# Kernel tuning notes

Hardware: AMD Instinct MI355X
Metric: run time of the kernel (lower is better)

## Reference

```python
import jax, jax.numpy as jnp
import numpy as np

LAMDA = 0.1    # regularization strength
ALPHA = 1.0    # proximal weighting (default forward arg)
TAU = 0.25     # Chambolle step size
MAX_ITER = 50
TOL = 1e-4


def _gradient(x):
    # forward differences with zero padding at the far boundary -> (2, H, W)
    gx = jnp.pad(x[1:, :] - x[:-1, :], ((0, 1), (0, 0)))
    gy = jnp.pad(x[:, 1:] - x[:, :-1], ((0, 0), (0, 1)))
    return jnp.stack((gx, gy), axis=0)


def _divergence(p):
    # matches torch: pad(p[:-1]-p[1:], 1 at the leading boundary)
    dx = jnp.pad(p[0][:-1, :] - p[0][1:, :], ((1, 0), (0, 0)))
    dy = jnp.pad(p[1][:, :-1] - p[1][:, 1:], ((0, 0), (1, 0)))
    return dx + dy


def setup_inputs() -> dict:
    key = jax.random.key(0)
    x = jax.random.normal(key, (4096, 4096), dtype=jnp.float32)
    return {"x": x}


def reference(x):
    def body(carry, _):
        p, done = carry
        g = _gradient(x - ALPHA * LAMDA * _divergence(p))
        p_new = jnp.clip(p + TAU * g, -1.0, 1.0)  # l1 norm projection
        dp_max = jnp.max(jnp.abs(p_new - p))
        # emulate the early break: freeze p once converged
        p_next = jnp.where(done, p, p_new)
        done = done | (dp_max < TOL)
        return (p_next, done), None

    p0 = jnp.zeros((2,) + x.shape, dtype=x.dtype)
    (p, _), _ = jax.lax.scan(body, (p0, jnp.array(False)), None, length=MAX_ITER)
    return x - ALPHA * LAMDA * _divergence(p)
```

## Files before the change

kernel.cpp:

```cpp
#include <hip/hip_runtime.h>
#include <hip/hip_fp16.h>

#define HH 4096
#define WW 4096

constexpr float C_LAM = 0.1f;
constexpr float TAU_F = 0.25f;

#define BX 64
#define BY 8
#define VEC 4
#define TILE_W (BX * VEC)

#define TW2 64
#define TH2 32
#define ERR 36
#define ECC 72
#define NCH (ECC / 4)
#define NSL (ERR * NCH)
#define LSZ (ERR * ECC)

#define TH8 32
#define TW8 64
#define XC8 80
#define NS8 12
#define NQ8 10
#define NT8 120

typedef float    __attribute__((ext_vector_type(4))) f32x4_t;
typedef float    __attribute__((ext_vector_type(2))) f32x2_t;
typedef unsigned __attribute__((ext_vector_type(2))) u32x2_t;

union H2x4 { float4 f4; f32x4_t v4; __half2 h2[4]; unsigned u32[4]; };
union H2x2 { float2 f2; f32x2_t v2; __half2 h2[2]; unsigned u32[2]; };
union H2U  { __half2 h; unsigned int u; };

__device__ __forceinline__ float clip1(float v) {
    return fminf(1.0f, fmaxf(-1.0f, v));
}

__device__ __forceinline__ unsigned h2u(__half2 h) { H2U a; a.h = h; return a.u; }
__device__ __forceinline__ __half2  u2h(unsigned u){ H2U a; a.u = u; return a.h; }

__device__ __forceinline__ __half2 permh(__half2 a, __half2 b, unsigned sel) {
    unsigned d;
    asm("v_perm_b32 %0, %1, %2, %3" : "=v"(d) : "v"(h2u(a)), "v"(h2u(b)), "v"(sel));
    return u2h(d);
}
__device__ __forceinline__ __half2 andh(__half2 v, unsigned m) { return u2h(h2u(v) & m); }

__device__ __forceinline__ __half2 clamp1h2(__half2 v) {
    H2U a; a.h = v;
    unsigned int lo = 0xBC00BC00u;
    unsigned int hi = 0x3C003C00u;
    unsigned int t, r;
    asm("v_pk_max_f16 %0, %1, %2" : "=v"(t) : "v"(a.u), "v"(lo));
    asm("v_pk_min_f16 %0, %1, %2" : "=v"(r) : "v"(t),   "v"(hi));
    H2U b; b.u = r;
    return b.h;
}

__device__ __forceinline__ __half2 shfl_up_h2(__half2 v) {
    H2U a; a.h = v;
    int s = __shfl_up((int)a.u, 1, 64);
    H2U b; b.u = (unsigned)s;
    return b.h;
}

__device__ __forceinline__ __half2 align16(__half2 hi, __half2 lo) {
    H2U a, b, d;
    a.h = hi; b.h = lo;
    asm("v_alignbit_b32 %0, %1, %2, 16" : "=v"(d.u) : "v"(a.u), "v"(b.u));
    return d.h;
}

__global__ __launch_bounds__(512) void tv_first(const float* __restrict__ x,
                                                __half2* __restrict__ po,
                                                __half* __restrict__ xh)
{
    const int tx = threadIdx.x, ty = threadIdx.y;
    const int i = blockIdx.y * BY + ty;
    const int j = blockIdx.x * TILE_W + tx * VEC;
    const size_t idx = (size_t)i * WW + j;

    float4 xc4 = *(const float4*)(x + idx);
    float4 xd4 = make_float4(0.f, 0.f, 0.f, 0.f);
    if (i < HH - 1) xd4 = *(const float4*)(x + idx + WW);

    float c[4] = {xc4.x, xc4.y, xc4.z, xc4.w};
    float d[4] = {xd4.x, xd4.y, xd4.z, xd4.w};

    float xr = __shfl_down(c[0], 1, 64);
    if (tx == BX - 1 && j + VEC < WW) xr = x[idx + VEC];

    H2x4 o;
#pragma unroll
    for (int e = 0; e < 4; ++e) {
        float gx = (i < HH - 1) ? (d[e] - c[e]) : 0.f;
        float rn = (e < 3) ? c[e + 1] : xr;
        float gy = (j + e < WW - 1) ? (rn - c[e]) : 0.f;
        o.h2[e] = __floats2half2_rn(clip1(TAU_F * gx), clip1(TAU_F * gy));
    }
    *(float4*)(po + idx) = o.f4;

    H2x2 xs;
    xs.h2[0] = __floats2half2_rn(c[0], c[1]);
    xs.h2[1] = __floats2half2_rn(c[2], c[3]);
    *(float2*)(xh + idx) = xs.f2;
}

template<bool EDGE>
__device__ __forceinline__ void iter8_body(const __half* __restrict__ xh,
                                           const __half2* __restrict__ pi,
                                           __half2* __restrict__ po,
                                           __half* pxB, __half* uT,
                                           unsigned* pyE, unsigned* uE)
{
    const int tid = threadIdx.x;
    const bool act = (tid < NT8);
    const int t = act ? tid : (NT8 - 1);
    const int s = t / NQ8;
    const int q = t - s * NQ8;
    const int r0 = blockIdx.y * TH8, c0 = blockIdx.x * TW8;
    const int gi0 = r0 - 8 + 4 * s;
    const int gj0 = c0 - 8 + 8 * q;
    const int gjc = EDGE ? min(max(gj0, 0), WW - 8) : gj0;

    const int lB  = s * XC8 + 8 * q;
    const int lBu = ((s > 0) ? (s - 1) : 0) * XC8 + 8 * q;
    const int lBd = ((s < NS8 - 1) ? (s + 1) : s) * XC8 + 8 * q;
    const int eO = t * 2;
    const int eL = ((q > 0) ? (t - 1) : t) * 2;
    const int eR = ((q < NQ8 - 1) ? (t + 1) : t) * 2;
    const bool wout = act && (s >= 2) && (s <= 9) && (q >= 1) && (q <= 8);

    unsigned mdy = 0xFFFFFFFFu, mgy = 0xFFFFFFFFu;
    if (EDGE) {
        if (gj0 == 0)      mdy = 0xFFFF0000u;
        if (gj0 + 8 == WW) mgy = 0x0000FFFFu;
    }

    const __half2 tau2 = __float2half2_rn(TAU_F);
    const __half2 nC2  = __float2half2_rn(-C_LAM);
    const unsigned SEL0 = 0x05040100u;
    const unsigned SELH = 0x07060302u;
    const unsigned SELM = 0x05040302u;

    __half2 X[4][4], Y[4][4], XHr[4][4], U[4][4];

#pragma unroll
    for (int k = 0; k < 4; ++k) {
        int gik = gi0 + k;
        if (EDGE) gik = min(max(gik, 0), HH - 1);
        const size_t go = (size_t)gik * WW + gjc;
        H2x4 v0; v0.v4 = *(const f32x4_t*)(pi + go);
        H2x4 v1; v1.v4 = *(const f32x4_t*)(pi + go + 4);
        H2x4 xv; xv.v4 = *(const f32x4_t*)(xh + go);
        X[k][0] = permh(v0.h2[1], v0.h2[0], SEL0);
        Y[k][0] = permh(v0.h2[1], v0.h2[0], SELH);
        X[k][1] = permh(v0.h2[3], v0.h2[2], SEL0);
        Y[k][1] = permh(v0.h2[3], v0.h2[2], SELH);
        X[k][2] = permh(v1.h2[1], v1.h2[0], SEL0);
        Y[k][2] = permh(v1.h2[1], v1.h2[0], SELH);
        X[k][3] = permh(v1.h2[3], v1.h2[2], SEL0);
        Y[k][3] = permh(v1.h2[3], v1.h2[2], SELH);
#pragma unroll
        for (int m = 0; m < 4; ++m) XHr[k][m] = xv.h2[m];
    }

    auto publish = [&]() {
        if (act) {
            H2x4 w;
#pragma unroll
            for (int m = 0; m < 4; ++m) w.h2[m] = X[3][m];
            *(f32x4_t*)(pxB + lB) = w.v4;
            u32x2_t e;
            e.x = h2u(permh(Y[1][3], Y[0][3], SELH));
            e.y = h2u(permh(Y[3][3], Y[2][3], SELH));
            *(u32x2_t*)(pyE + eO) = e;
        }
    };

    auto ustage = [&]() {
        H2x4 pu; pu.v4 = *(const f32x4_t*)(pxB + lBu);
        u32x2_t Lp = *(const u32x2_t*)(pyE + eL);
        const __half2 L0 = u2h(Lp.x), L1 = u2h(Lp.y);
#pragma unroll
        for (int k = 0; k < 4; ++k) {
            __half2 dx[4], zm[4], dy[4];
#pragma unroll
            for (int m = 0; m < 4; ++m)
                dx[m] = __hsub2((k == 0) ? pu.h2[m] : X[k - 1][m], X[k][m]);
            if (EDGE && !(gi0 + k > 0)) {
#pragma unroll
                for (int m = 0; m < 4; ++m) dx[m] = u2h(0u);
            }
            zm[0] = (k == 0) ? permh(Y[k][0], L0, SEL0)
                  : (k == 1) ? permh(Y[k][0], L0, SELM)
                  : (k == 2) ? permh(Y[k][0], L1, SEL0)
                             : permh(Y[k][0], L1, SELM);
            zm[1] = align16(Y[k][1], Y[k][0]);
            zm[2] = align16(Y[k][2], Y[k][1]);
            zm[3] = align16(Y[k][3], Y[k][2]);
#pragma unroll
            for (int m = 0; m < 4; ++m) dy[m] = __hsub2(zm[m], Y[k][m]);
            if (EDGE) dy[0] = andh(dy[0], mdy);
#pragma unroll
            for (int m = 0; m < 4; ++m)
                U[k][m] = __hfma2(__hadd2(dx[m], dy[m]), nC2, XHr[k][m]);
        }
        if (act) {
            H2x4 w;
#pragma unroll
            for (int m = 0; m < 4; ++m) w.h2[m] = U[0][m];
            *(f32x4_t*)(uT + lB) = w.v4;
            u32x2_t e;
            e.x = h2u(permh(U[1][0], U[0][0], SEL0));
            e.y = h2u(permh(U[3][0], U[2][0], SEL0));
            *(u32x2_t*)(uE + eO) = e;
        }
    };

    auto pstage = [&]() {
        H2x4 ud; ud.v4 = *(const f32x4_t*)(uT + lBd);
        u32x2_t Rp = *(const u32x2_t*)(uE + eR);
        const __half2 R0 = u2h(Rp.x), R1 = u2h(Rp.y);
#pragma unroll
        for (int k = 0; k < 4; ++k) {
            __half2 gx[4], zp[4], gy[4];
#pragma unroll
            for (int m = 0; m < 4; ++m)
                gx[m] = __hsub2((k == 3) ? ud.h2[m] : U[k + 1][m], U[k][m]);
            if (EDGE && !(gi0 + k < HH - 1)) {
#pragma unroll
                for (int m = 0; m < 4; ++m) gx[m] = u2h(0u);
            }
            zp[0] = align16(U[k][1], U[k][0]);
            zp[1] = align16(U[k][2], U[k][1]);
            zp[2] = align16(U[k][3], U[k][2]);
            zp[3] = (k == 0) ? permh(R0, U[k][3], SELM)
                  : (k == 1) ? permh(R0, U[k][3], SELH)
                  : (k == 2) ? permh(R1, U[k][3], SELM)
                             : permh(R1, U[k][3], SELH);
#pragma unroll
            for (int m = 0; m < 4; ++m) gy[m] = __hsub2(zp[m], U[k][m]);
            if (EDGE) gy[3] = andh(gy[3], mgy);
#pragma unroll
            for (int m = 0; m < 4; ++m) {
                X[k][m] = clamp1h2(__hfma2(gx[m], tau2, X[k][m]));
                Y[k][m] = clamp1h2(__hfma2(gy[m], tau2, Y[k][m]));
            }
        }
    };

#pragma unroll 1
    for (int it = 0; it < 7; ++it) {
        publish(); __syncthreads();
        ustage();  __syncthreads();
        pstage();
    }
    publish(); __syncthreads();
    ustage();  __syncthreads();
    pstage();

    if (wout) {
#pragma unroll
        for (int k = 0; k < 4; ++k) {
            const size_t go = (size_t)(gi0 + k) * WW + gj0;
            H2x4 w0, w1;
            w0.h2[0] = permh(Y[k][0], X[k][0], SEL0);
            w0.h2[1] = permh(Y[k][0], X[k][0], SELH);
            w0.h2[2] = permh(Y[k][1], X[k][1], SEL0);
            w0.h2[3] = permh(Y[k][1], X[k][1], SELH);
            w1.h2[0] = permh(Y[k][2], X[k][2], SEL0);
            w1.h2[1] = permh(Y[k][2], X[k][2], SELH);
            w1.h2[2] = permh(Y[k][3], X[k][3], SEL0);
            w1.h2[3] = permh(Y[k][3], X[k][3], SELH);
            *(f32x4_t*)(po + go)     = w0.v4;
            *(f32x4_t*)(po + go + 4) = w1.v4;
        }
    }
}

__global__ __launch_bounds__(128, 4) void tv_iter8(const __half* __restrict__ xh,
                                                   const __half2* __restrict__ pi,
                                                   __half2* __restrict__ po)
{
    __shared__ __align__(16) __half   pxB[NS8 * XC8];
    __shared__ __align__(16) __half   uT [NS8 * XC8];
    __shared__ __align__(8)  unsigned pyE[NT8 * 2];
    __shared__ __align__(8)  unsigned uE [NT8 * 2];

    const bool edge = (blockIdx.x == 0) || (blockIdx.x == gridDim.x - 1) ||
                      (blockIdx.y == 0) || (blockIdx.y == gridDim.y - 1);
    if (!edge) iter8_body<false>(xh, pi, po, pxB, uT, pyE, uE);
    else       iter8_body<true >(xh, pi, po, pxB, uT, pyE, uE);
}

__global__ __launch_bounds__(256) void tv_last(const __half* __restrict__ xh,
                                               const float* __restrict__ x,
                                               const __half2* __restrict__ pi,
                                               float* __restrict__ out)
{
    __shared__ __half2 sp0[LSZ];
    __shared__ __half2 sp1[LSZ];
    __shared__ float   su [LSZ];

    const int tid  = threadIdx.x;
    const int lane = tid & 63;
    const int r0 = blockIdx.y * TH2;
    const int c0 = blockIdx.x * TW2;
    const __half2 tau2 = __float2half2_rn(TAU_F);

    int lb[3], lup[3], llf[3], ldn[3], lrt[3], gj0a[3], gofs[3];
    bool wr[3];
#pragma unroll
    for (int r = 0; r < 3; ++r) {
        int slot = tid + 256 * r;
        wr[r] = (slot < NSL);
        if (slot >= NSL) slot = NSL - 1;
        int cr = slot / NCH;
        int cc = slot - cr * NCH;
        int gi  = r0 - 2 + cr;
        int gj0 = c0 - 4 + cc * 4;
        int gic = min(max(gi, 0), HH - 1);
        int gjc = min(max(gj0, 0), WW - 4);
        gofs[r] = gic * WW + gjc;
        int l   = cr * ECC + cc * 4;
        lb[r]  = l;
        lup[r] = (cr > 0) ? l - ECC : l;
        llf[r] = (l > 0) ? l - 1 : 0;
        ldn[r] = (cr < ERR - 1) ? l + ECC : l;
        lrt[r] = min(l + 4, LSZ - 1);
        gj0a[r] = gj0;
    }

    __half2 c2[3][4];
    H2x2    xc[3];
#pragma unroll
    for (int r = 0; r < 3; ++r) {
        H2x4 v; v.f4 = *(const float4*)(pi + gofs[r]);
        xc[r].f2    = *(const float2*)(xh + gofs[r]);
        if (wr[r]) *(float4*)&sp0[lb[r]] = v.f4;
        c2[r][0] = v.h2[0]; c2[r][1] = v.h2[1];
        c2[r][2] = v.h2[2]; c2[r][3] = v.h2[3];
    }
    __syncthreads();

    float u1v[3][4];
#pragma unroll
    for (int r = 0; r < 3; ++r) {
        H2x4 up; up.f4 = *(float4*)&sp0[lup[r]];
        __half2 lf = shfl_up_h2(c2[r][3]);
        if (lane == 0) lf = sp0[llf[r]];
        float xs[4] = {__low2float(xc[r].h2[0]), __high2float(xc[r].h2[0]),
                       __low2float(xc[r].h2[1]), __high2float(xc[r].h2[1])};
        float4 w;
        float* wp = &w.x;
#pragma unroll
        for (int e = 0; e < 4; ++e) {
            __half2 cc = c2[r][e];
            __half2 le = (e == 0) ? lf : c2[r][e - 1];
            float dx = __low2float(up.h2[e]) - __low2float(cc);
            float dy = __high2float(le) - __high2float(cc);
            dy = (gj0a[r] + e > 0) ? dy : 0.f;
            float u = xs[e] - C_LAM * (dx + dy);
            u1v[r][e] = u;
            wp[e] = u;
        }
        if (wr[r]) *(float4*)&su[lb[r]] = w;
    }
    __syncthreads();

#pragma unroll
    for (int r = 0; r < 3; ++r) {
        float4 dn4 = *(float4*)&su[ldn[r]];
        float urr = __shfl_down(u1v[r][0], 1, 64);
        if (lane == 63) urr = su[lrt[r]];
        float dn[4] = {dn4.x, dn4.y, dn4.z, dn4.w};
        H2x4 w;
#pragma unroll
        for (int e = 0; e < 4; ++e) {
            float uc = u1v[r][e];
            float gx = dn[e] - uc;
            float rt = (e == 3) ? urr : u1v[r][e + 1];
            float gy = (gj0a[r] + e < WW - 1) ? (rt - uc) : 0.f;
            __half2 g = __float22half2_rn(make_float2(gx, gy));
            w.h2[e] = clamp1h2(__hfma2(g, tau2, c2[r][e]));
        }
        if (wr[r]) *(float4*)&sp1[lb[r]] = w.f4;
    }
    __syncthreads();

#pragma unroll
    for (int r = 0; r < 2; ++r) {
        int slot = tid + 256 * r;
        int ir = slot >> 4, icc = slot & 15;
        int er = ir + 2, ec = icc * 4 + 4;
        int l  = er * ECC + ec;
        int gi = r0 + ir, gj = c0 + icc * 4;

        H2x4 pc_; pc_.f4 = *(float4*)&sp1[l];
        H2x4 pu_; pu_.f4 = *(float4*)&sp1[l - ECC];
        __half2 plf = shfl_up_h2(pc_.h2[3]);
        if ((tid & 15) == 0) plf = sp1[l - 1];

        float4 xr4 = *(const float4*)(x + (size_t)gi * WW + gj);
        float xv[4] = {xr4.x, xr4.y, xr4.z, xr4.w};
        float o[4];
#pragma unroll
        for (int e = 0; e < 4; ++e) {
            __half2 cc = pc_.h2[e];
            __half2 le = (e == 0) ? plf : pc_.h2[e - 1];
            float dx = __low2float(pu_.h2[e]) - __low2float(cc);
            dx = (gi > 0) ? dx : 0.f;
            float dy = __high2float(le) - __high2float(cc);
            dy = (gj + e > 0) ? dy : 0.f;
            o[e] = xv[e] - C_LAM * (dx + dy);
        }
        *(float4*)(out + (size_t)gi * WW + gj) = make_float4(o[0], o[1], o[2], o[3]);
    }
}

extern "C" void kernel_launch(void* const* d_in, const int* in_sizes, int n_in,
                              void* d_out, int out_size, void* d_ws, size_t ws_size,
                              hipStream_t stream)
{
    const float* x = (const float*)d_in[0];
    float* out = (float*)d_out;
    const size_t N = (size_t)HH * (size_t)WW;

    __half2* pA = (__half2*)d_ws;
    __half2* pB = pA + N;
    __half*  xh = (__half*)(pB + N);

    dim3 b1(BX, BY), g1(WW / TILE_W, HH / BY);
    dim3 b8(128),    g8(WW / TW8, HH / TH8);
    dim3 bL(256),    gL(WW / TW2, HH / TH2);

    tv_first<<<g1, b1, 0, stream>>>(x, pA, xh);
    __half2 *pin = pA, *pout = pB;
    for (int p = 0; p < 6; ++p) {
        tv_iter8<<<g8, b8, 0, stream>>>(xh, pin, pout);
        __half2* t = pin; pin = pout; pout = t;
    }
    tv_last<<<gL, bL, 0, stream>>>(xh, x, pin, out);
}
```

Before: 506.0 us.

## Halve rows per thread in fused 8-iteration kernel, doubling block threads

Each thread of the temporally-blocked 8-iteration kernel now owns 2 rows instead of 4, so the block grows from 128 to 256 threads (240 active), with shared edge buffers shrunk to one word per thread. The goal is to cut per-thread register pressure and expose more parallel waves per tile to hide latency. In exchange there are more shared-memory halo exchanges relative to compute, and the occupancy hint in launch bounds is dropped.

```diff
diff --git a/kernel.cpp b/kernel.cpp
--- a/kernel.cpp
+++ b/kernel.cpp
@@ -23,13 +23,12 @@
 #define TH8 32
 #define TW8 64
 #define XC8 80
-#define NS8 12
+#define NS8 24
 #define NQ8 10
-#define NT8 120
+#define NT8 240
 
 typedef float    __attribute__((ext_vector_type(4))) f32x4_t;
 typedef float    __attribute__((ext_vector_type(2))) f32x2_t;
-typedef unsigned __attribute__((ext_vector_type(2))) u32x2_t;
 
 union H2x4 { float4 f4; f32x4_t v4; __half2 h2[4]; unsigned u32[4]; };
 union H2x2 { float2 f2; f32x2_t v2; __half2 h2[2]; unsigned u32[2]; };
@@ -122,17 +121,17 @@
     const int s = t / NQ8;
     const int q = t - s * NQ8;
     const int r0 = blockIdx.y * TH8, c0 = blockIdx.x * TW8;
-    const int gi0 = r0 - 8 + 4 * s;
+    const int gi0 = r0 - 8 + 2 * s;
     const int gj0 = c0 - 8 + 8 * q;
     const int gjc = EDGE ? min(max(gj0, 0), WW - 8) : gj0;
 
     const int lB  = s * XC8 + 8 * q;
     const int lBu = ((s > 0) ? (s - 1) : 0) * XC8 + 8 * q;
     const int lBd = ((s < NS8 - 1) ? (s + 1) : s) * XC8 + 8 * q;
-    const int eO = t * 2;
-    const int eL = ((q > 0) ? (t - 1) : t) * 2;
-    const int eR = ((q < NQ8 - 1) ? (t + 1) : t) * 2;
-    const bool wout = act && (s >= 2) && (s <= 9) && (q >= 1) && (q <= 8);
+    const int eO = t;
+    const int eL = (q > 0) ? (t - 1) : t;
+    const int eR = (q < NQ8 - 1) ? (t + 1) : t;
+    const bool wout = act && (s >= 4) && (s < 20) && (q >= 1) && (q <= 8);
 
     unsigned mdy = 0xFFFFFFFFu, mgy = 0xFFFFFFFFu;
     if (EDGE) {
@@ -146,10 +145,10 @@
     const unsigned SELH = 0x07060302u;
     const unsigned SELM = 0x05040302u;
 
-    __half2 X[4][4], Y[4][4], XHr[4][4], U[4][4];
-
-#pragma unroll
-    for (int k = 0; k < 4; ++k) {
+    __half2 X[2][4], Y[2][4], XHr[2][4], U[2][4];
+
+#pragma unroll
+    for (int k = 0; k < 2; ++k) {
         int gik = gi0 + k;
         if (EDGE) gik = min(max(gik, 0), HH - 1);
         const size_t go = (size_t)gik * WW + gjc;
@@ -172,33 +171,27 @@
         if (act) {
             H2x4 w;
 #pragma unroll
-            for (int m = 0; m < 4; ++m) w.h2[m] = X[3][m];
+            for (int m = 0; m < 4; ++m) w.h2[m] = X[1][m];
             *(f32x4_t*)(pxB + lB) = w.v4;
-            u32x2_t e;
-            e.x = h2u(permh(Y[1][3], Y[0][3], SELH));
-            e.y = h2u(permh(Y[3][3], Y[2][3], SELH));
-            *(u32x2_t*)(pyE + eO) = e;
+            pyE[eO] = h2u(permh(Y[1][3], Y[0][3], SELH));
         }
     };
 
     auto ustage = [&]() {
         H2x4 pu; pu.v4 = *(const f32x4_t*)(pxB + lBu);
-        u32x2_t Lp = *(const u32x2_t*)(pyE + eL);
-        const __half2 L0 = u2h(Lp.x), L1 = u2h(Lp.y);
-#pragma unroll
-        for (int k = 0; k < 4; ++k) {
+        const __half2 L = u2h(pyE[eL]);
+#pragma unroll
+        for (int k = 0; k < 2; ++k) {
             __half2 dx[4], zm[4], dy[4];
 #pragma unroll
             for (int m = 0; m < 4; ++m)
-                dx[m] = __hsub2((k == 0) ? pu.h2[m] : X[k - 1][m], X[k][m]);
+                dx[m] = __hsub2((k == 0) ? pu.h2[m] : X[0][m], X[k][m]);
             if (EDGE && !(gi0 + k > 0)) {
 #pragma unroll
                 for (int m = 0; m < 4; ++m) dx[m] = u2h(0u);
             }
-            zm[0] = (k == 0) ? permh(Y[k][0], L0, SEL0)
-                  : (k == 1) ? permh(Y[k][0], L0, SELM)
-                  : (k == 2) ? permh(Y[k][0], L1, SEL0)
-                             : permh(Y[k][0], L1, SELM);
+            zm[0] = (k == 0) ? permh(Y[k][0], L, SEL0)
+                             : permh(Y[k][0], L, SELM);
             zm[1] = align16(Y[k][1], Y[k][0]);
             zm[2] = align16(Y[k][2], Y[k][1]);
             zm[3] = align16(Y[k][3], Y[k][2]);
@@ -214,23 +207,19 @@
 #pragma unroll
             for (int m = 0; m < 4; ++m) w.h2[m] = U[0][m];
             *(f32x4_t*)(uT + lB) = w.v4;
-            u32x2_t e;
-            e.x = h2u(permh(U[1][0], U[0][0], SEL0));
-            e.y = h2u(permh(U[3][0], U[2][0], SEL0));
-            *(u32x2_t*)(uE + eO) = e;
+            uE[eO] = h2u(permh(U[1][0], U[0][0], SEL0));
         }
     };
 
     auto pstage = [&]() {
         H2x4 ud; ud.v4 = *(const f32x4_t*)(uT + lBd);
-        u32x2_t Rp = *(const u32x2_t*)(uE + eR);
-        const __half2 R0 = u2h(Rp.x), R1 = u2h(Rp.y);
-#pragma unroll
-        for (int k = 0; k < 4; ++k) {
+        const __half2 R = u2h(uE[eR]);
+#pragma unroll
+        for (int k = 0; k < 2; ++k) {
             __half2 gx[4], zp[4], gy[4];
 #pragma unroll
             for (int m = 0; m < 4; ++m)
-                gx[m] = __hsub2((k == 3) ? ud.h2[m] : U[k + 1][m], U[k][m]);
+                gx[m] = __hsub2((k == 1) ? ud.h2[m] : U[1][m], U[k][m]);
             if (EDGE && !(gi0 + k < HH - 1)) {
 #pragma unroll
                 for (int m = 0; m < 4; ++m) gx[m] = u2h(0u);
@@ -238,10 +227,8 @@
             zp[0] = align16(U[k][1], U[k][0]);
             zp[1] = align16(U[k][2], U[k][1]);
             zp[2] = align16(U[k][3], U[k][2]);
-            zp[3] = (k == 0) ? permh(R0, U[k][3], SELM)
-                  : (k == 1) ? permh(R0, U[k][3], SELH)
-                  : (k == 2) ? permh(R1, U[k][3], SELM)
-                             : permh(R1, U[k][3], SELH);
+            zp[3] = (k == 0) ? permh(R, U[k][3], SELM)
+                             : permh(R, U[k][3], SELH);
 #pragma unroll
             for (int m = 0; m < 4; ++m) gy[m] = __hsub2(zp[m], U[k][m]);
             if (EDGE) gy[3] = andh(gy[3], mgy);
@@ -265,7 +252,7 @@
 
     if (wout) {
 #pragma unroll
-        for (int k = 0; k < 4; ++k) {
+        for (int k = 0; k < 2; ++k) {
             const size_t go = (size_t)(gi0 + k) * WW + gj0;
             H2x4 w0, w1;
             w0.h2[0] = permh(Y[k][0], X[k][0], SEL0);
@@ -282,14 +269,14 @@
     }
 }
 
-__global__ __launch_bounds__(128, 4) void tv_iter8(const __half* __restrict__ xh,
-                                                   const __half2* __restrict__ pi,
-                                                   __half2* __restrict__ po)
+__global__ __launch_bounds__(256) void tv_iter8(const __half* __restrict__ xh,
+                                                const __half2* __restrict__ pi,
+                                                __half2* __restrict__ po)
 {
     __shared__ __align__(16) __half   pxB[NS8 * XC8];
     __shared__ __align__(16) __half   uT [NS8 * XC8];
-    __shared__ __align__(8)  unsigned pyE[NT8 * 2];
-    __shared__ __align__(8)  unsigned uE [NT8 * 2];
+    __shared__ __align__(8)  unsigned pyE[NT8];
+    __shared__ __align__(8)  unsigned uE [NT8];
 
     const bool edge = (blockIdx.x == 0) || (blockIdx.x == gridDim.x - 1) ||
                       (blockIdx.y == 0) || (blockIdx.y == gridDim.y - 1);
@@ -435,7 +422,7 @@
     __half*  xh = (__half*)(pB + N);
 
     dim3 b1(BX, BY), g1(WW / TILE_W, HH / BY);
-    dim3 b8(128),    g8(WW / TW8, HH / TH8);
+    dim3 b8(256),    g8(WW / TW8, HH / TH8);
     dim3 bL(256),    gL(WW / TW2, HH / TH2);
 
     tv_first<<<g1, b1, 0, stream>>>(x, pA, xh);
```

After: 476.3 us. -5.9%, faster.
